# Performance work log

Hardware: AMD Instinct MI355X
Metric: run time of the kernel (lower is better)

Reference implementation:

```python
import jax, jax.numpy as jnp
import numpy as np

B, D = 256, 8                 # trees, tree depth (leaves at level D)
V, E, H = 32000, 128, 128     # vocab, embedding_dim, hidden_dim
N = 2 ** (D + 1) - 1          # 511 heap-indexed nodes per tree


def setup_inputs() -> dict:
    key = jax.random.key(0)
    ks = jax.random.split(key, 9)
    s = 0.05  # keep gate pre-activations in a sane range
    return {
        "tokens": jax.random.randint(ks[0], (B, N), 0, V),
        "arity": jax.random.randint(ks[1], (B, 2 ** D - 1), 0, 2).astype(jnp.int32),
        "emb": jax.random.normal(ks[2], (V, E), dtype=jnp.float32) * s,
        "W": jax.random.normal(ks[3], (4, E, H), dtype=jnp.float32) * s,      # i,f,o,u
        "bW": jax.random.normal(ks[4], (4, H), dtype=jnp.float32) * s,
        "Ubin": jax.random.normal(ks[5], (5, 2 * H, H), dtype=jnp.float32) * s,  # i,f_l,f_r,o,u
        "bUbin": jax.random.normal(ks[6], (5, H), dtype=jnp.float32) * s,
        "Uun": jax.random.normal(ks[7], (4, H, H), dtype=jnp.float32) * s,    # i,f,o,u
        "bUun": jax.random.normal(ks[8], (4, H), dtype=jnp.float32) * s,
    }


def reference(tokens, arity, emb, W, bW, Ubin, bUbin, Uun, bUun):
    # Level-synchronous bottom-up Tree-LSTM over heap-indexed perfect trees.
    x = emb[tokens]  # [B, N, E] embedding gather for every node
    depth = int(np.log2(tokens.shape[1] + 1)) - 1

    # Leaves (level `depth`): h = tanh(W_u x + b_u), c = 0
    off = 2 ** depth - 1
    lx = x[:, off:]  # [B, 2^D, E]
    h = jnp.tanh(jnp.einsum('bne,eh->bnh', lx, W[3]) + bW[3])
    c = jnp.zeros_like(h)

    for l in range(depth - 1, -1, -1):
        o2, cnt = 2 ** l - 1, 2 ** l
        nx = x[:, o2:o2 + cnt]            # [B, cnt, E] this level's tokens
        h_l, h_r = h[:, ::2], h[:, 1::2]   # children (heap order)
        c_l, c_r = c[:, ::2], c[:, 1::2]

        # Shared input projections for all 4 gates, fused into one GEMM
        Wx = jnp.einsum('bne,geh->gbnh', nx, W) + bW[:, None, None, :]
        hcat = jnp.concatenate([h_l, h_r], axis=-1)  # [B, cnt, 2H]
        Ub = jnp.einsum('bnk,gkh->gbnh', hcat, Ubin) + bUbin[:, None, None, :]
        Uu = jnp.einsum('bnh,gha->gbna', h_l, Uun) + bUun[:, None, None, :]

        # Binary branch: i, f_l, f_r (shared W_f), o, u
        i_b = jax.nn.sigmoid(Wx[0] + Ub[0])
        f_lg = jax.nn.sigmoid(Wx[1] + Ub[1])
        f_rg = jax.nn.sigmoid(Wx[1] + Ub[2])
        o_b = jax.nn.sigmoid(Wx[2] + Ub[3])
        u_b = jnp.tanh(Wx[3] + Ub[4])
        c_b = i_b * u_b + f_lg * c_l + f_rg * c_r
        h_b = o_b * jnp.tanh(c_b)

        # Unary branch (child = left child)
        i_u = jax.nn.sigmoid(Wx[0] + Uu[0])
        f_u = jax.nn.sigmoid(Wx[1] + Uu[1])
        o_u = jax.nn.sigmoid(Wx[2] + Uu[2])
        u_u = jnp.tanh(Wx[3] + Uu[3])
        c_u = i_u * u_u + f_u * c_l
        h_u = o_u * jnp.tanh(c_u)

        m = (arity[:, o2:o2 + cnt] == 1)[..., None]  # True -> binary node
        h = jnp.where(m, h_b, h_u)
        c = jnp.where(m, c_b, c_u)

    return h[:, 0], c[:, 0]  # root (h, c), each [B, H]
```

## Files before the change

### kernel.cpp

```cpp
#include <hip/hip_runtime.h>
#include <hip/hip_bf16.h>

#define NTOK 511
#define NINT 255

typedef unsigned short u16;
typedef __attribute__((ext_vector_type(8))) short bf16x8;
typedef __attribute__((ext_vector_type(4))) float f32x4;

constexpr int OFF_FLAG = 0;
constexpr int OFF_WB   = 4;
constexpr int W3B = 294912;
constexpr int WB_ELEMS = 311296;
constexpr int OFF_BIAS = OFF_WB + WB_ELEMS / 2;
constexpr int BW4 = 0, BUB4 = 512, BUB1 = 1024, BUU4 = 1152, B3 = 1664;
constexpr int BIAS_FLOATS = 1792;
constexpr int OFF_ROOT  = OFF_BIAS + BIAS_FLOATS;
constexpr int OFF_CHUNK = OFF_ROOT + 65536;
constexpr long PER_TREE = 49152;

__device__ __forceinline__ float bf2f(__hip_bfloat16 v) { return __bfloat162float(v); }
__device__ __forceinline__ short f2s(float f) {
    __hip_bfloat16 b = __float2bfloat16(f);
    return *reinterpret_cast<short*>(&b);
}
__device__ __forceinline__ float sigm(float x) { return 1.0f / (1.0f + __expf(-x)); }
__device__ __forceinline__ float tanh_(float x) { return 1.0f - 2.0f / (__expf(2.0f * x) + 1.0f); }

__device__ __forceinline__ float ldf(const void* p, long idx, int isbf) {
    return isbf ? bf2f(((const __hip_bfloat16*)p)[idx]) : ((const float*)p)[idx];
}

__device__ __forceinline__ bf16x8 ldA(const void* p, long idx, int isbf) {
    if (isbf) return *(const bf16x8*)((const short*)p + idx);
    const float* f = (const float*)p + idx;
    float4 a = *(const float4*)f, b = *(const float4*)(f + 4);
    bf16x8 r;
    r[0] = f2s(a.x); r[1] = f2s(a.y); r[2] = f2s(a.z); r[3] = f2s(a.w);
    r[4] = f2s(b.x); r[5] = f2s(b.y); r[6] = f2s(b.z); r[7] = f2s(b.w);
    return r;
}

typedef const __attribute__((address_space(1))) unsigned int* gp1_t;
typedef __attribute__((address_space(3))) unsigned int* lp3_t;
__device__ __forceinline__ void stage16(const void* g, void* l) {
    __builtin_amdgcn_global_load_lds((gp1_t)g, (lp3_t)l, 16, 0, 0);
}

__global__ void detect_kernel(const void* W, float* ws) {
    if (threadIdx.x == 0 && blockIdx.x == 0) {
        const u16* u = (const u16*)W;
        int cnt = 0;
        for (int i = 0; i < 128; i += 2) {
            u16 x = u[i];
            int ex = (x >> 7) & 0xff;
            if (x == 0 || (ex >= 96 && ex <= 127)) cnt++;
        }
        ((int*)ws)[0] = (cnt >= 48) ? 1 : 0;
    }
}

__global__ __launch_bounds__(256) void repack_mfma(
    const void* W, const void* bW, const void* Ubin, const void* bUbin,
    const void* Uun, const void* bUun, float* ws)
{
    const int isbf = ((const int*)ws)[0];
    short* wb = (short*)(ws + OFF_WB);
    float* bias = ws + OFF_BIAS;
    int tid = blockIdx.x * blockDim.x + threadIdx.x;
    int nth = gridDim.x * blockDim.x;

    for (int idx = tid; idx < 294912; idx += nth) {
        int e = idx & 511, fjc = idx >> 9;
        int jc = fjc / 72, f = fjc - jc * 72;
        int lane = e >> 3, id8 = e & 7;
        int j = jc * 16 + (lane & 15);
        float v;
        if (f < 16) {
            int g = f >> 2, ks = f & 3;
            int k = ks * 32 + (lane >> 4) * 8 + id8;
            v = ldf(W, (long)g * 16384 + k * 128 + j, isbf);
        } else if (f < 32) {
            int fu = f - 16; int g = fu >> 2, ks = fu & 3;
            int k = ks * 32 + (lane >> 4) * 8 + id8;
            v = ldf(Uun, (long)g * 16384 + k * 128 + j, isbf);
        } else {
            int fb = f - 32; int g = fb >> 3, ks = fb & 7;
            int k = ks * 32 + (lane >> 4) * 8 + id8;
            v = ldf(Ubin, (long)g * 32768 + k * 128 + j, isbf);
        }
        wb[idx] = f2s(v);
    }
    for (int idx = tid; idx < 16384; idx += nth) {
        int e = idx & 511, frag = idx >> 9;
        int jc = frag >> 2, ks = frag & 3;
        int lane = e >> 3, id8 = e & 7;
        int k = ks * 32 + (lane >> 4) * 8 + id8;
        int j = jc * 16 + (lane & 15);
        wb[W3B + idx] = f2s(ldf(W, (long)3 * 16384 + k * 128 + j, isbf));
    }
    for (int j = tid; j < 128; j += nth) {
        float4 b;
        b.x = ldf(bW, 0 * 128 + j, isbf); b.y = ldf(bW, 1 * 128 + j, isbf);
        b.z = ldf(bW, 2 * 128 + j, isbf); b.w = ldf(bW, 3 * 128 + j, isbf);
        ((float4*)(bias + BW4))[j] = b;
        float4 bb;
        bb.x = ldf(bUbin, 0 * 128 + j, isbf); bb.y = ldf(bUbin, 1 * 128 + j, isbf);
        bb.z = ldf(bUbin, 2 * 128 + j, isbf); bb.w = ldf(bUbin, 3 * 128 + j, isbf);
        ((float4*)(bias + BUB4))[j] = bb;
        (bias + BUB1)[j] = ldf(bUbin, 4 * 128 + j, isbf);
        float4 bu;
        bu.x = ldf(bUun, 0 * 128 + j, isbf); bu.y = ldf(bUun, 1 * 128 + j, isbf);
        bu.z = ldf(bUun, 2 * 128 + j, isbf); bu.w = ldf(bUun, 3 * 128 + j, isbf);
        ((float4*)(bias + BUU4))[j] = bu;
        (bias + B3)[j] = ldf(bW, 3 * 128 + j, isbf);
    }
}

#define MFMA(A, B, C) __builtin_amdgcn_mfma_f32_16x16x32_bf16(A, B, C, 0, 0, 0)

__global__ __launch_bounds__(256, 2) void leaf_mfma(
    const int* __restrict__ tokens, const void* emb, const float* __restrict__ ws,
    short* __restrict__ hOut, int treeOff, int Mtot, int iters)
{
    __shared__ short hst[4][16][132];
    const int t = threadIdx.x;
    const int isbf = ((const int*)ws)[0];
    const int wv = t >> 6, lane = t & 63, quad = lane >> 4, l16 = lane & 15;
    const short* wb = (const short*)(ws + OFF_WB);
    const float* bias = ws + OFF_BIAS;

    bf16x8 bf[32];
#pragma unroll
    for (int f = 0; f < 32; ++f)
        bf[f] = *(const bf16x8*)(wb + W3B + f * 512 + lane * 8);
    float b3v[8];
#pragma unroll
    for (int jc = 0; jc < 8; ++jc) b3v[jc] = (bias + B3)[jc * 16 + l16];

    for (int it = 0; it < iters; ++it) {
        int rb = (blockIdx.x * iters + it) * 64 + wv * 16;
        if (rb >= Mtot) break;
        int p = rb + l16; if (p >= Mtot) p = Mtot - 1;
        int bl = p >> 8, i = p & 255;
        int tk = tokens[(long)(treeOff + bl) * NTOK + 255 + i];
        bf16x8 ax[4];
#pragma unroll
        for (int ks = 0; ks < 4; ++ks)
            ax[ks] = ldA(emb, (long)tk * 128 + ks * 32 + quad * 8, isbf);
        f32x4 acc[8];
#pragma unroll
        for (int jc = 0; jc < 8; ++jc) acc[jc] = {0.f, 0.f, 0.f, 0.f};
#pragma unroll
        for (int jc = 0; jc < 8; ++jc)
#pragma unroll
            for (int ks = 0; ks < 4; ++ks)
                acc[jc] = MFMA(ax[ks], bf[jc * 4 + ks], acc[jc]);
#pragma unroll
        for (int jc = 0; jc < 8; ++jc)
#pragma unroll
            for (int r = 0; r < 4; ++r)
                hst[wv][quad * 4 + r][jc * 16 + l16] = f2s(tanh_(acc[jc][r] + b3v[jc]));
        int nloc = lane >> 2, c0 = (lane & 3) * 4;
        int prow = rb + nloc;
        if (prow < Mtot) {
#pragma unroll
            for (int jcb = 0; jcb < 8; ++jcb) {
                uint2 v = *(const uint2*)&hst[wv][nloc][jcb * 16 + c0];
                *(uint2*)&hOut[((long)jcb * Mtot + prow) * 16 + c0] = v;
            }
        }
    }
}

__global__ __launch_bounds__(512, 4) void level8_mfma(
    const int* __restrict__ tokens, const int* __restrict__ arity, const void* emb,
    const float* __restrict__ ws, const short* __restrict__ hChild,
    const float* __restrict__ cChild, short* __restrict__ hOut, float* __restrict__ cOut,
    float* __restrict__ rootH, float* __restrict__ rootC,
    int lvl, int treeOff, int leafchild, int isRoot, int Mtot, int Mchild,
    int NBMB, int Q)
{
    __shared__ short Bs[72 * 512];
    __shared__ short hst[8][16][20];

    const int t = threadIdx.x;
    const int isbf = ((const int*)ws)[0];
    const int jc = blockIdx.x / NBMB;
    const int mb = blockIdx.x - jc * NBMB;
    const int wv = t >> 6, lane = t & 63, quad = lane >> 4, l16 = lane & 15;
    const int cnt = 1 << lvl, o2 = cnt - 1;
    const short* wb = (const short*)(ws + OFF_WB);
    const float* bias = ws + OFF_BIAS;
    const short* wj = wb + (long)jc * 36864;
    const int j = jc * 16 + l16;

#pragma unroll
    for (int s = 0; s < 9; ++s) {
        int off = (s * 512 + t) * 8;
        stage16(wj + off, Bs + off);
    }
    __syncthreads();

    for (int q = 0; q < Q; ++q) {
        const int p0 = (mb * Q + q) * 128;
        if (p0 >= Mtot) break;

        int row = wv * 16 + l16;
        int p = p0 + row; if (p >= Mtot) p = Mtot - 1;
        int bl = p >> lvl, i = p - (bl << lvl);
        long crow = (long)bl * (cnt << 1) + 2 * i;
        int tk = tokens[(long)(treeOff + bl) * NTOK + o2 + i];
        bf16x8 ax[4], ah[8];
#pragma unroll
        for (int ks = 0; ks < 4; ++ks)
            ax[ks] = ldA(emb, (long)tk * 128 + ks * 32 + quad * 8, isbf);
#pragma unroll
        for (int ks = 0; ks < 8; ++ks) {
            int k0 = ks * 32 + quad * 8;
            int side = k0 >> 7, kl = k0 & 127;
            ah[ks] = *(const bf16x8*)(hChild +
                ((long)(kl >> 4) * Mchild + crow + side) * 16 + (kl & 15));
        }

        float clv[4], crv[4];
#pragma unroll
        for (int r = 0; r < 4; ++r) {
            if (!leafchild) {
                int pe = p0 + wv * 16 + quad * 4 + r;
                if (pe >= Mtot) pe = Mtot - 1;
                int ble = pe >> lvl, ie = pe - (ble << lvl);
                long crowe = (long)ble * (cnt << 1) + 2 * ie;
                clv[r] = cChild[((long)jc * Mchild + crowe) * 16 + l16];
                crv[r] = cChild[((long)jc * Mchild + crowe + 1) * 16 + l16];
            } else { clv[r] = 0.f; crv[r] = 0.f; }
        }

        f32x4 aW[4], aU[4], aB[5];
#pragma unroll
        for (int g = 0; g < 4; ++g) { aW[g] = {0,0,0,0}; aU[g] = {0,0,0,0}; }
#pragma unroll
        for (int g = 0; g < 5; ++g) aB[g] = {0,0,0,0};

#pragma unroll
        for (int f = 0; f < 16; ++f) {
            bf16x8 b = *(const bf16x8*)&Bs[f * 512 + lane * 8];
            aW[f >> 2] = MFMA(ax[f & 3], b, aW[f >> 2]);
        }
#pragma unroll
        for (int f = 16; f < 32; ++f) {
            bf16x8 b = *(const bf16x8*)&Bs[f * 512 + lane * 8];
            aU[(f - 16) >> 2] = MFMA(ah[(f - 16) & 3], b, aU[(f - 16) >> 2]);
        }
#pragma unroll
        for (int f = 32; f < 72; ++f) {
            bf16x8 b = *(const bf16x8*)&Bs[f * 512 + lane * 8];
            int fb = f - 32;
            aB[fb >> 3] = MFMA(ah[fb & 7], b, aB[fb >> 3]);
        }

        const float4 bw = ((const float4*)(bias + BW4))[j];
        const float4 bb = ((const float4*)(bias + BUB4))[j];
        const float  b1 = (bias + BUB1)[j];
        const float4 bu = ((const float4*)(bias + BUU4))[j];

#pragma unroll
        for (int r = 0; r < 4; ++r) {
            int ml = wv * 16 + quad * 4 + r;
            int pr = p0 + ml;
            bool val = (pr < Mtot);
            int pc = val ? pr : Mtot - 1;
            int ble = pc >> lvl, ie = pc - (ble << lvl);
            int arvv = arity[(long)(treeOff + ble) * NINT + o2 + ie];
            bool bin = (arvv == 1);
            float w0 = aW[0][r] + bw.x;
            float w1 = aW[1][r] + bw.y;
            float w2 = aW[2][r] + bw.z;
            float w3 = aW[3][r] + bw.w;
            float pi, pf, po, pu;
            if (bin) { pi = w0 + aB[0][r] + bb.x; pf = w1 + aB[1][r] + bb.y;
                       po = w2 + aB[3][r] + bb.w; pu = w3 + aB[4][r] + b1; }
            else     { pi = w0 + aU[0][r] + bu.x; pf = w1 + aU[1][r] + bu.y;
                       po = w2 + aU[2][r] + bu.z; pu = w3 + aU[3][r] + bu.w; }
            float cl = clv[r];
            float cr = bin ? crv[r] : 0.f;
            float frv = bin ? sigm(w1 + aB[2][r] + bb.z) : 0.f;
            float ig = sigm(pi), fg = sigm(pf), og = sigm(po), ug = tanh_(pu);
            float c = ig * ug + fg * cl + frv * cr;
            float h = og * tanh_(c);
            if (isRoot) {
                if (val) {
                    rootH[(long)(treeOff + ble) * 128 + j] = h;
                    rootC[(long)(treeOff + ble) * 128 + j] = c;
                }
            } else {
                if (val) cOut[((long)jc * Mtot + pc) * 16 + l16] = c;
                hst[wv][quad * 4 + r][l16] = f2s(h);
            }
        }
        if (!isRoot) {
            int nloc = lane >> 2, c0 = (lane & 3) * 4;
            int prow = p0 + wv * 16 + nloc;
            if (prow < Mtot) {
                uint2 v = *(const uint2*)&hst[wv][nloc][c0];
                *(uint2*)&hOut[((long)jc * Mtot + prow) * 16 + c0] = v;
            }
        }
    }
}

__global__ __launch_bounds__(256) void out_kernel(const float* ws, void* out)
{
    const int isbf = ((const int*)ws)[0];
    const float* rootH = ws + OFF_ROOT;
    const float* rootC = rootH + 32768;
    int t = blockIdx.x * 256 + threadIdx.x;
    float h = rootH[t], c = rootC[t];
    if (isbf) {
        ((__hip_bfloat16*)out)[t]         = __float2bfloat16(h);
        ((__hip_bfloat16*)out)[32768 + t] = __float2bfloat16(c);
    } else {
        ((float*)out)[t]         = h;
        ((float*)out)[32768 + t] = c;
    }
}

extern "C" void kernel_launch(void* const* d_in, const int* in_sizes, int n_in,
                              void* d_out, int out_size, void* d_ws, size_t ws_size,
                              hipStream_t stream)
{
    const int* tokens = (const int*)d_in[0];
    const int* arity  = (const int*)d_in[1];
    const void* emb   = d_in[2];
    const void* W     = d_in[3];
    const void* bW    = d_in[4];
    const void* Ubin  = d_in[5];
    const void* bUbin = d_in[6];
    const void* Uun   = d_in[7];
    const void* bUun  = d_in[8];

    float* ws = (float*)d_ws;

    int Bc = 256;
    while (Bc > 1 && (size_t)(OFF_CHUNK + Bc * PER_TREE) * 4 > ws_size) Bc >>= 1;
    const int nCh = 256 / Bc;

    detect_kernel<<<1, 64, 0, stream>>>(W, ws);
    repack_mfma<<<128, 256, 0, stream>>>(W, bW, Ubin, bUbin, Uun, bUun, ws);

    short* Ha = (short*)(ws + OFF_CHUNK);
    short* Hb = Ha + (long)Bc * 32768;
    float* Ca = (float*)(Hb + (long)Bc * 16384);
    float* Cb = Ca + (long)Bc * 8192;
    float* rootH = ws + OFF_ROOT;
    float* rootC = rootH + 32768;

    for (int cidx = 0; cidx < nCh; ++cidx) {
        int toff = cidx * Bc;
        {
            int Mleaf = Bc * 256;
            int NBL = (Mleaf + 63) / 64; if (NBL > 512) NBL = 512;
            int itersL = (Mleaf + NBL * 64 - 1) / (NBL * 64);
            leaf_mfma<<<NBL, 256, 0, stream>>>(tokens, emb, ws, Ha, toff, Mleaf, itersL);
        }
        for (int l = 7; l >= 0; --l) {
            int M = Bc << l;
            int Mchild = Bc << (l + 1);
            const short* hC = (l & 1) ? Ha : Hb;
            const float* cC = (l & 1) ? Ca : Cb;
            short* hO = (l & 1) ? Hb : Ha;
            float* cO = (l & 1) ? Cb : Ca;
            int lc = (l == 7) ? 1 : 0;
            int isRoot = (l == 0) ? 1 : 0;
            int NBM = (M + 127) / 128;
            int Q = NBM / 64; if (Q < 1) Q = 1;
            int NBMB = (NBM + Q - 1) / Q;
            level8_mfma<<<dim3(NBMB * 8), 512, 0, stream>>>(
                tokens, arity, emb, ws, hC, cC, hO, cO, rootH, rootC,
                l, toff, lc, isRoot, M, Mchild, NBMB, Q);
        }
    }
    out_kernel<<<128, 256, 0, stream>>>(ws, d_out);
}
```

Baseline: 172.1 us.

## Store child hidden states in MFMA-fragment-ready layout to simplify parent loads

Hidden-state outputs are now written straight to global memory in a tiled layout that matches the A-fragment order the parent level's MFMA consumes. This drops the LDS staging buffers and turns the parent's scattered child loads into contiguous 16-byte per-lane loads. The cost is scalar 2-byte scattered global stores in place of the previous coalesced 8-byte stores. It also assumes Mchild is padded to whole 16-row tiles.

```diff
diff --git a/kernel.cpp b/kernel.cpp
--- a/kernel.cpp
+++ b/kernel.cpp
@@ -18,6 +18,7 @@
 constexpr int OFF_ROOT  = OFF_BIAS + BIAS_FLOATS;
 constexpr int OFF_CHUNK = OFF_ROOT + 65536;
 constexpr long PER_TREE = 49152;
+
 
 __device__ __forceinline__ float bf2f(__hip_bfloat16 v) { return __bfloat162float(v); }
 __device__ __forceinline__ short f2s(float f) {
@@ -119,11 +120,18 @@
 
 #define MFMA(A, B, C) __builtin_amdgcn_mfma_f32_16x16x32_bf16(A, B, C, 0, 0, 0)
 
+__device__ __forceinline__ void stH(short* __restrict__ hOut, int cn, int j, short hs) {
+    int pp = cn >> 1;
+    int k0 = (cn & 1) * 128 + j;
+    long addr = (((long)(pp >> 4) * 8 + (k0 >> 5)) << 9)
+              + ((((k0 >> 3) & 3) * 16 + (pp & 15)) << 3) + (k0 & 7);
+    hOut[addr] = hs;
+}
+
 __global__ __launch_bounds__(256, 2) void leaf_mfma(
     const int* __restrict__ tokens, const void* emb, const float* __restrict__ ws,
     short* __restrict__ hOut, int treeOff, int Mtot, int iters)
 {
-    __shared__ short hst[4][16][132];
     const int t = threadIdx.x;
     const int isbf = ((const int*)ws)[0];
     const int wv = t >> 6, lane = t & 63, quad = lane >> 4, l16 = lane & 15;
@@ -159,17 +167,10 @@
 #pragma unroll
         for (int jc = 0; jc < 8; ++jc)
 #pragma unroll
-            for (int r = 0; r < 4; ++r)
-                hst[wv][quad * 4 + r][jc * 16 + l16] = f2s(tanh_(acc[jc][r] + b3v[jc]));
-        int nloc = lane >> 2, c0 = (lane & 3) * 4;
-        int prow = rb + nloc;
-        if (prow < Mtot) {
-#pragma unroll
-            for (int jcb = 0; jcb < 8; ++jcb) {
-                uint2 v = *(const uint2*)&hst[wv][nloc][jcb * 16 + c0];
-                *(uint2*)&hOut[((long)jcb * Mtot + prow) * 16 + c0] = v;
+            for (int r = 0; r < 4; ++r) {
+                int cn = rb + quad * 4 + r;
+                stH(hOut, cn, jc * 16 + l16, f2s(tanh_(acc[jc][r] + b3v[jc])));
             }
-        }
     }
 }
 
@@ -182,7 +183,6 @@
     int NBMB, int Q)
 {
     __shared__ short Bs[72 * 512];
-    __shared__ short hst[8][16][20];
 
     const int t = threadIdx.x;
     const int isbf = ((const int*)ws)[0];
@@ -209,19 +209,15 @@
         int row = wv * 16 + l16;
         int p = p0 + row; if (p >= Mtot) p = Mtot - 1;
         int bl = p >> lvl, i = p - (bl << lvl);
-        long crow = (long)bl * (cnt << 1) + 2 * i;
         int tk = tokens[(long)(treeOff + bl) * NTOK + o2 + i];
         bf16x8 ax[4], ah[8];
 #pragma unroll
         for (int ks = 0; ks < 4; ++ks)
             ax[ks] = ldA(emb, (long)tk * 128 + ks * 32 + quad * 8, isbf);
-#pragma unroll
-        for (int ks = 0; ks < 8; ++ks) {
-            int k0 = ks * 32 + quad * 8;
-            int side = k0 >> 7, kl = k0 & 127;
-            ah[ks] = *(const bf16x8*)(hChild +
-                ((long)(kl >> 4) * Mchild + crow + side) * 16 + (kl & 15));
-        }
+        const short* hT = hChild + (((long)(p0 >> 4) + wv) << 12);
+#pragma unroll
+        for (int ks = 0; ks < 8; ++ks)
+            ah[ks] = *(const bf16x8*)(hT + ks * 512 + lane * 8);
 
         float clv[4], crv[4];
 #pragma unroll
@@ -293,17 +289,9 @@
                     rootH[(long)(treeOff + ble) * 128 + j] = h;
                     rootC[(long)(treeOff + ble) * 128 + j] = c;
                 }
-            } else {
-                if (val) cOut[((long)jc * Mtot + pc) * 16 + l16] = c;
-                hst[wv][quad * 4 + r][l16] = f2s(h);
-            }
-        }
-        if (!isRoot) {
-            int nloc = lane >> 2, c0 = (lane & 3) * 4;
-            int prow = p0 + wv * 16 + nloc;
-            if (prow < Mtot) {
-                uint2 v = *(const uint2*)&hst[wv][nloc][c0];
-                *(uint2*)&hOut[((long)jc * Mtot + prow) * 16 + c0] = v;
+            } else if (val) {
+                cOut[((long)jc * Mtot + pc) * 16 + l16] = c;
+                stH(hOut, pc, j, f2s(h));
             }
         }
     }
```

New measurement: 169.8 us. No clear change (-1.3%).
